# Optimization experiments

Hardware: AMD Instinct MI355X
Metric: run time of the kernel (lower is better)

## Reference

```python
import jax, jax.numpy as jnp
import numpy as np

N_NODES = 100000
N_EDGES = 3200000
IN_DIM = 512
HID_DIM = 16


def spmm(edge_src, edge_dst, edge_weight, feats):
    # out[i] = sum_{(j->i) in E} w_e * feats[j]  (sparse adj @ feats)
    gathered = feats[edge_src] * edge_weight[:, None]  # [E, D]
    return jax.ops.segment_sum(gathered, edge_dst, num_segments=N_NODES)


def setup_inputs() -> dict:
    key = jax.random.key(0)
    ks = jax.random.split(key, 8)
    x = jax.random.normal(ks[0], (N_NODES, IN_DIM), dtype=jnp.float32)
    edge_src = jax.random.randint(ks[1], (N_EDGES,), 0, N_NODES, dtype=jnp.int32)
    edge_dst = jax.random.randint(ks[2], (N_EDGES,), 0, N_NODES, dtype=jnp.int32)
    # normalized adjacency weights (positive, small, like D^-1/2 A D^-1/2 entries)
    edge_weight = jax.random.uniform(ks[3], (N_EDGES,), dtype=jnp.float32) * 0.1
    # Glorot-style init for GraphConvolution weights
    W1 = jax.random.normal(ks[4], (IN_DIM, HID_DIM), dtype=jnp.float32) * (1.0 / np.sqrt(IN_DIM))
    b1 = jnp.zeros((HID_DIM,), dtype=jnp.float32)
    W2 = jax.random.normal(ks[5], (HID_DIM, 1), dtype=jnp.float32) * (1.0 / np.sqrt(HID_DIM))
    b2 = jnp.zeros((1,), dtype=jnp.float32)
    return {"x": x, "edge_src": edge_src, "edge_dst": edge_dst,
            "edge_weight": edge_weight, "W1": W1, "b1": b1, "W2": W2, "b2": b2}


def reference(x, edge_src, edge_dst, edge_weight, W1, b1, W2, b2):
    # Layer 1: GraphConvolution(input_dim -> hidden_dim) + ReLU
    h = spmm(edge_src, edge_dst, edge_weight, x @ W1) + b1  # [N, 16]
    h = jax.nn.relu(h)
    # dropout is identity in eval mode (training=False)
    # Layer 2: GraphConvolution(hidden_dim -> 1)
    out = spmm(edge_src, edge_dst, edge_weight, h @ W2) + b2  # [N, 1]
    return out
```

## Files before the change

kernel.cpp:

```cpp
#include <hip/hip_runtime.h>
#include <hip/hip_fp16.h>

#define N_NODES 100000
#define N_EDGES 3200000
#define IN_DIM  512
#define HID_DIM 16

#define B_BKT   782
#define BKT_SH  7
#define EPB2    5000
#define NBLK2   640
#define CAP_MAX 4608

#define G1_TILES 6250

typedef __attribute__((ext_vector_type(8))) short bf16x8;
typedef __attribute__((ext_vector_type(4))) float f32x4;

__device__ __forceinline__ void atomic_add_f32(float* p, float v) {
    __hip_atomic_fetch_add(p, v, __ATOMIC_RELAXED, __HIP_MEMORY_SCOPE_AGENT);
}
__device__ __forceinline__ int atomic_add_i32(int* p, int v) {
    return __hip_atomic_fetch_add(p, v, __ATOMIC_RELAXED, __HIP_MEMORY_SCOPE_AGENT);
}

__device__ __forceinline__ unsigned short bf16_rne(float f) {
    unsigned u = __float_as_uint(f);
    return (unsigned short)((u + 0x7fffu + ((u >> 16) & 1u)) >> 16);
}

__global__ void z0_init(int* __restrict__ cursor, int cap) {
    int b = blockIdx.x * blockDim.x + threadIdx.x;
    if (b < B_BKT) cursor[b] = b * cap;
}

__global__ __launch_bounds__(256) void g1_xw_mfma(const float* __restrict__ x,
                                                  const float* __restrict__ W1,
                                                  __half* __restrict__ xwh) {
    __shared__ alignas(16) unsigned short whi[16 * 64 * 8];
    __shared__ alignas(16) unsigned short wlo[16 * 64 * 8];
    const int t = threadIdx.x;

    for (int idx = t; idx < 16 * 64 * 8; idx += 256) {
        int c  = idx >> 9;
        int l  = (idx >> 3) & 63;
        int tt = idx & 7;
        int k  = c * 32 + ((l >> 4) << 3) + tt;
        int j  = l & 15;
        float w = W1[k * HID_DIM + j];
        unsigned u = __float_as_uint(w);
        float hif = __uint_as_float(u & 0xffff0000u);
        whi[idx] = (unsigned short)(u >> 16);
        wlo[idx] = bf16_rne(w - hif);
    }
    __syncthreads();

    const int lane = t & 63;
    const int wid  = blockIdx.x * 4 + (t >> 6);
    if (wid >= G1_TILES) return;
    const int row0 = wid * 16;

    const float* xrow = x + (size_t)(row0 + (lane & 15)) * IN_DIM + ((lane >> 4) << 3);
    const unsigned short* whp = &whi[lane * 8];
    const unsigned short* wlp = &wlo[lane * 8];

    f32x4 acc = {0.f, 0.f, 0.f, 0.f};
    float4 p0[2], p1[2];
    p0[0] = *(const float4*)(xrow);
    p1[0] = *(const float4*)(xrow + 4);
    p0[1] = *(const float4*)(xrow + 32);
    p1[1] = *(const float4*)(xrow + 36);
#pragma unroll
    for (int c = 0; c < 16; ++c) {
        const int cur = c & 1;
        float4 n0, n1;
        if (c < 14) {
            n0 = *(const float4*)(xrow + (c + 2) * 32);
            n1 = *(const float4*)(xrow + (c + 2) * 32 + 4);
        }
        float av[8] = {p0[cur].x, p0[cur].y, p0[cur].z, p0[cur].w,
                       p1[cur].x, p1[cur].y, p1[cur].z, p1[cur].w};
        bf16x8 ah, al;
#pragma unroll
        for (int e = 0; e < 8; ++e) {
            unsigned u = __float_as_uint(av[e]);
            ah[e] = (short)(u >> 16);
            float lof = av[e] - __uint_as_float(u & 0xffff0000u);
            al[e] = (short)bf16_rne(lof);
        }
        bf16x8 bh = *(const bf16x8*)(whp + (size_t)c * 512);
        bf16x8 bl = *(const bf16x8*)(wlp + (size_t)c * 512);
        acc = __builtin_amdgcn_mfma_f32_16x16x32_bf16(ah, bh, acc, 0, 0, 0);
        acc = __builtin_amdgcn_mfma_f32_16x16x32_bf16(al, bh, acc, 0, 0, 0);
        acc = __builtin_amdgcn_mfma_f32_16x16x32_bf16(ah, bl, acc, 0, 0, 0);
        if (c < 14) { p0[cur] = n0; p1[cur] = n1; }
    }

    const int n     = lane & 15;
    const int rbase = row0 + ((lane >> 4) << 2);
#pragma unroll
    for (int i = 0; i < 4; ++i)
        xwh[(size_t)(rbase + i) * HID_DIM + n] = __float2half_rn(acc[i]);
}

__global__ __launch_bounds__(512) void s1_bin2(const int* __restrict__ src,
                                               const int* __restrict__ dst,
                                               const float* __restrict__ wgt,
                                               int* __restrict__ cursor,
                                               uint2* __restrict__ rec, int cap) {
    __shared__ uint2 srt[EPB2];
    __shared__ unsigned short bkt[EPB2];
    __shared__ int hist[B_BKT];
    __shared__ int lbase[B_BKT];
    __shared__ int gbase[B_BKT];
    __shared__ int scn[512];
    const int t = threadIdx.x;
    for (int b = t; b < B_BKT; b += 512) hist[b] = 0;
    __syncthreads();

    const int e0 = blockIdx.x * EPB2;
    const int4*   d4 = (const int4*)(dst + e0);
    const int4*   s4 = (const int4*)(src + e0);
    const float4* w4 = (const float4*)(wgt + e0);
    const int NG = EPB2 / 4;

    for (int g = t; g < NG; g += 512) {
        int4 d = d4[g];
        atomicAdd(&hist[d.x >> BKT_SH], 1);
        atomicAdd(&hist[d.y >> BKT_SH], 1);
        atomicAdd(&hist[d.z >> BKT_SH], 1);
        atomicAdd(&hist[d.w >> BKT_SH], 1);
    }
    __syncthreads();

    int c0 = 0, c1 = 0;
    if (t < 391) { c0 = hist[2 * t]; c1 = hist[2 * t + 1]; }
    int s = c0 + c1;
    scn[t] = s;
    __syncthreads();
    for (int off = 1; off < 512; off <<= 1) {
        int v = (t >= off) ? scn[t - off] : 0;
        __syncthreads();
        scn[t] += v;
        __syncthreads();
    }
    int excl = scn[t] - s;
    if (t < 391) {
        lbase[2 * t]     = excl;
        lbase[2 * t + 1] = excl + c0;
    }
    __syncthreads();

    for (int b = t; b < B_BKT; b += 512) {
        int c = hist[b];
        gbase[b] = c > 0 ? atomic_add_i32(&cursor[b], c) : 0;
    }
    __syncthreads();
    for (int b = t; b < B_BKT; b += 512) hist[b] = lbase[b];
    __syncthreads();

    for (int g = t; g < NG; g += 512) {
        int4 d = d4[g];
        int4 sv = s4[g];
        float4 w = w4[g];
        {
            int b = d.x >> BKT_SH;
            int pos = atomicAdd(&hist[b], 1);
            srt[pos] = make_uint2(((unsigned)sv.x << BKT_SH) | (unsigned)(d.x & 127),
                                  __float_as_uint(w.x));
            bkt[pos] = (unsigned short)b;
        }
        {
            int b = d.y >> BKT_SH;
            int pos = atomicAdd(&hist[b], 1);
            srt[pos] = make_uint2(((unsigned)sv.y << BKT_SH) | (unsigned)(d.y & 127),
                                  __float_as_uint(w.y));
            bkt[pos] = (unsigned short)b;
        }
        {
            int b = d.z >> BKT_SH;
            int pos = atomicAdd(&hist[b], 1);
            srt[pos] = make_uint2(((unsigned)sv.z << BKT_SH) | (unsigned)(d.z & 127),
                                  __float_as_uint(w.z));
            bkt[pos] = (unsigned short)b;
        }
        {
            int b = d.w >> BKT_SH;
            int pos = atomicAdd(&hist[b], 1);
            srt[pos] = make_uint2(((unsigned)sv.w << BKT_SH) | (unsigned)(d.w & 127),
                                  __float_as_uint(w.w));
            bkt[pos] = (unsigned short)b;
        }
    }
    __syncthreads();

    for (int i = t; i < EPB2; i += 512) {
        int b = bkt[i];
        rec[gbase[b] + (i - lbase[b])] = srt[i];
    }
}

__global__ __launch_bounds__(512) void s2p4(const int* __restrict__ cursor,
                                            uint2* __restrict__ rec,
                                            int2* __restrict__ row,
                                            const __half* __restrict__ xwh,
                                            const float* __restrict__ b1,
                                            const float* __restrict__ W2,
                                            float* __restrict__ hw, int cap) {
    __shared__ uint2 srt[CAP_MAX];
    __shared__ int ocnt[128], scn[128], cur[128];
    const int t = threadIdx.x;
    const int bkt = blockIdx.x;
    const int e0 = bkt * cap;
    int n = cursor[bkt] - e0;
    n = max(0, min(n, cap));
    if (t < 128) ocnt[t] = 0;
    __syncthreads();
    for (int i = t; i < n; i += 512)
        atomicAdd(&ocnt[rec[e0 + i].x & 127u], 1);
    __syncthreads();
    if (t < 128) scn[t] = ocnt[t];
    __syncthreads();
    for (int off = 1; off < 128; off <<= 1) {
        int v = 0;
        if (t < 128 && t >= off) v = scn[t - off];
        __syncthreads();
        if (t < 128 && t >= off) scn[t] += v;
        __syncthreads();
    }
    if (t < 128) {
        int b = scn[t] - ocnt[t];
        cur[t] = b;
        int node = (bkt << BKT_SH) + t;
        if (node < N_NODES) row[node] = make_int2(e0 + b, ocnt[t]);
    }
    __syncthreads();
    for (int i = t; i < n; i += 512) {
        uint2 r = rec[e0 + i];
        int d = (int)(r.x & 127u);
        int pos = atomicAdd(&cur[d], 1);
        srt[pos] = make_uint2(r.x >> BKT_SH, r.y);
    }
    __syncthreads();
    for (int i = t; i < n; i += 512) rec[e0 + i] = srt[i];
    const int j = t & 15;
    for (int g = (t >> 4); g < 128; g += 32) {
        const int node = (bkt << BKT_SH) + g;
        if (node >= N_NODES) continue;
        int e = scn[g] - ocnt[g];
        const int end = scn[g];
        float acc = 0.0f;
        for (; e + 4 <= end; e += 4) {
            uint2 q0 = srt[e], q1 = srt[e + 1], q2 = srt[e + 2], q3 = srt[e + 3];
            float f0 = __half2float(xwh[(size_t)q0.x * HID_DIM + j]);
            float f1 = __half2float(xwh[(size_t)q1.x * HID_DIM + j]);
            float f2 = __half2float(xwh[(size_t)q2.x * HID_DIM + j]);
            float f3 = __half2float(xwh[(size_t)q3.x * HID_DIM + j]);
            acc += __uint_as_float(q0.y) * f0;
            acc += __uint_as_float(q1.y) * f1;
            acc += __uint_as_float(q2.y) * f2;
            acc += __uint_as_float(q3.y) * f3;
        }
        for (; e < end; ++e) {
            uint2 q = srt[e];
            acc += __uint_as_float(q.y) * __half2float(xwh[(size_t)q.x * HID_DIM + j]);
        }
        float v = fmaxf(acc + b1[j], 0.0f) * W2[j];
        v += __shfl_xor(v, 1);
        v += __shfl_xor(v, 2);
        v += __shfl_xor(v, 4);
        v += __shfl_xor(v, 8);
        if (j == 0) hw[node] = v;
    }
}

__global__ __launch_bounds__(256) void p5_layer2(const int2* __restrict__ row,
                                                 const uint2* __restrict__ rec,
                                                 const float* __restrict__ hwv,
                                                 const float* __restrict__ b2,
                                                 float* __restrict__ out) {
    const int t = threadIdx.x;
    const int node = blockIdx.x * 32 + (t >> 3);
    const int i = t & 7;
    int2 r = row[node];
    const int end = r.x + r.y;
    int k = r.x + i;
    float s = 0.0f;
    for (; k + 24 < end; k += 32) {
        uint2 a = rec[k], b = rec[k + 8], c = rec[k + 16], d = rec[k + 24];
        float ha = hwv[a.x], hb = hwv[b.x], hc = hwv[c.x], hd = hwv[d.x];
        s += __uint_as_float(a.y) * ha + __uint_as_float(b.y) * hb
           + __uint_as_float(c.y) * hc + __uint_as_float(d.y) * hd;
    }
    for (; k < end; k += 8) {
        uint2 a = rec[k];
        s += __uint_as_float(a.y) * hwv[a.x];
    }
    s += __shfl_xor(s, 1);
    s += __shfl_xor(s, 2);
    s += __shfl_xor(s, 4);
    if (i == 0) out[node] = b2[0] + s;
}

__global__ void f0_zero(float* __restrict__ h, const float* __restrict__ b2,
                        float* __restrict__ out) {
    int i = blockIdx.x * blockDim.x + threadIdx.x;
    if (i < N_NODES * HID_DIM) h[i] = 0.0f;
    if (i < N_NODES) out[i] = b2[0];
}
__global__ void k2_spmm1(const int* __restrict__ src, const int* __restrict__ dst,
                         const float* __restrict__ wgt, const __half* __restrict__ xwh,
                         float* __restrict__ h) {
    int t = blockIdx.x * blockDim.x + threadIdx.x;
    int e = t >> 4;
    int j = t & (HID_DIM - 1);
    if (e < N_EDGES) {
        float v = wgt[e] * __half2float(xwh[(size_t)src[e] * HID_DIM + j]);
        atomic_add_f32(&h[(size_t)dst[e] * HID_DIM + j], v);
    }
}
__global__ void k3_act(const float* __restrict__ h, const float* __restrict__ b1,
                       const float* __restrict__ W2, float* __restrict__ hw) {
    int i = blockIdx.x * blockDim.x + threadIdx.x;
    if (i >= N_NODES) return;
    const float4* h4 = (const float4*)(h + (size_t)i * HID_DIM);
    const float4* b4 = (const float4*)b1;
    const float4* w4 = (const float4*)W2;
    float acc = 0.0f;
#pragma unroll
    for (int q = 0; q < HID_DIM / 4; ++q) {
        float4 hv = h4[q]; float4 bv = b4[q]; float4 wv = w4[q];
        acc += fmaxf(hv.x + bv.x, 0.0f) * wv.x;
        acc += fmaxf(hv.y + bv.y, 0.0f) * wv.y;
        acc += fmaxf(hv.z + bv.z, 0.0f) * wv.z;
        acc += fmaxf(hv.w + bv.w, 0.0f) * wv.w;
    }
    hw[i] = acc;
}
__global__ void k4_spmm2(const int* __restrict__ src, const int* __restrict__ dst,
                         const float* __restrict__ wgt, const float* __restrict__ hw,
                         float* __restrict__ out) {
    int e = blockIdx.x * blockDim.x + threadIdx.x;
    if (e < N_EDGES) atomic_add_f32(&out[dst[e]], wgt[e] * hw[src[e]]);
}


extern "C" void kernel_launch(void* const* d_in, const int* in_sizes, int n_in,
                              void* d_out, int out_size, void* d_ws, size_t ws_size,
                              hipStream_t stream) {
    const float* x    = (const float*)d_in[0];
    const int*   esrc = (const int*)  d_in[1];
    const int*   edst = (const int*)  d_in[2];
    const float* ew   = (const float*)d_in[3];
    const float* W1   = (const float*)d_in[4];
    const float* b1   = (const float*)d_in[5];
    const float* W2   = (const float*)d_in[6];
    const float* b2   = (const float*)d_in[7];
    float* out = (float*)d_out;
    char* ws = (char*)d_ws;

    __half* xwh    = (__half*)ws;
    float*  hw     = (float*)(ws + (size_t)N_NODES * HID_DIM * 2);
    int*    cursor = (int*)(hw + N_NODES);
    int2*   row    = (int2*)(((size_t)(cursor + B_BKT) + 7) & ~(size_t)7);
    size_t rec_off = ((size_t)((char*)(row + N_NODES) - ws) + 15) & ~(size_t)15;
    uint2* rec = (uint2*)(ws + rec_off);

    int cap = 0;
    if (ws_size > rec_off) {
        size_t cap_fit = (ws_size - rec_off) / ((size_t)B_BKT * sizeof(uint2));
        cap = (int)(cap_fit < CAP_MAX ? cap_fit : CAP_MAX);
    }

    if (cap >= 4480) {
        z0_init<<<(B_BKT + 255) / 256, 256, 0, stream>>>(cursor, cap);
        g1_xw_mfma<<<(G1_TILES + 3) / 4, 256, 0, stream>>>(x, W1, xwh);
        s1_bin2<<<NBLK2, 512, 0, stream>>>(esrc, edst, ew, cursor, rec, cap);
        s2p4<<<B_BKT, 512, 0, stream>>>(cursor, rec, row, xwh, b1, W2, hw, cap);
        p5_layer2<<<N_NODES / 32, 256, 0, stream>>>(row, rec, hw, b2, out);
    } else {
        __half* f_xwh = (__half*)ws;
        float*  f_h   = (float*)(ws + (size_t)N_NODES * HID_DIM * 2);
        float*  f_hw  = f_h + (size_t)N_NODES * HID_DIM;
        int n = N_NODES * HID_DIM;
        f0_zero<<<(n + 255) / 256, 256, 0, stream>>>(f_h, b2, out);
        g1_xw_mfma<<<(G1_TILES + 3) / 4, 256, 0, stream>>>(x, W1, f_xwh);
        k2_spmm1<<<(N_EDGES * 16) / 256, 256, 0, stream>>>(esrc, edst, ew, f_xwh, f_h);
        k3_act<<<(N_NODES + 255) / 256, 256, 0, stream>>>(f_h, b1, W2, f_hw);
        k4_spmm2<<<(N_EDGES + 255) / 256, 256, 0, stream>>>(esrc, edst, ew, f_hw, out);
    }
}
```

Measured before the change: 406.6 us.

## Merge X·W1 MFMA GEMM and edge binning into one heterogeneous launch

```diff
diff --git a/kernel.cpp b/kernel.cpp
--- a/kernel.cpp
+++ b/kernel.cpp
@@ -13,6 +13,8 @@
 #define CAP_MAX 4608
 
 #define G1_TILES 6250
+#define G1_BLK   782
+#define MERGED_SMEM 61440
 
 typedef __attribute__((ext_vector_type(8))) short bf16x8;
 typedef __attribute__((ext_vector_type(4))) float f32x4;
@@ -32,6 +34,175 @@
 __global__ void z0_init(int* __restrict__ cursor, int cap) {
     int b = blockIdx.x * blockDim.x + threadIdx.x;
     if (b < B_BKT) cursor[b] = b * cap;
+}
+
+__global__ __launch_bounds__(512) void m1_gs(const float* __restrict__ x,
+                                             const float* __restrict__ W1,
+                                             __half* __restrict__ xwh,
+                                             const int* __restrict__ src,
+                                             const int* __restrict__ dst,
+                                             const float* __restrict__ wgt,
+                                             int* __restrict__ cursor,
+                                             uint2* __restrict__ rec, int cap) {
+    extern __shared__ __align__(16) char smem[];
+    const int t = threadIdx.x;
+
+    if (blockIdx.x < NBLK2) {
+        uint2*          srt   = (uint2*)smem;
+        unsigned short* bkt   = (unsigned short*)(smem + 40000);
+        int*            hist  = (int*)(smem + 50000);
+        int*            lbase = (int*)(smem + 53128);
+        int*            gbase = (int*)(smem + 56256);
+        int*            scn   = (int*)(smem + 59384);
+
+        for (int b = t; b < B_BKT; b += 512) hist[b] = 0;
+        __syncthreads();
+
+        const int e0 = blockIdx.x * EPB2;
+        const int4*   d4 = (const int4*)(dst + e0);
+        const int4*   s4 = (const int4*)(src + e0);
+        const float4* w4 = (const float4*)(wgt + e0);
+        const int NG = EPB2 / 4;
+
+        for (int g = t; g < NG; g += 512) {
+            int4 d = d4[g];
+            atomicAdd(&hist[d.x >> BKT_SH], 1);
+            atomicAdd(&hist[d.y >> BKT_SH], 1);
+            atomicAdd(&hist[d.z >> BKT_SH], 1);
+            atomicAdd(&hist[d.w >> BKT_SH], 1);
+        }
+        __syncthreads();
+
+        int c0 = 0, c1 = 0;
+        if (t < 391) { c0 = hist[2 * t]; c1 = hist[2 * t + 1]; }
+        int s = c0 + c1;
+        scn[t] = s;
+        __syncthreads();
+        for (int off = 1; off < 512; off <<= 1) {
+            int v = (t >= off) ? scn[t - off] : 0;
+            __syncthreads();
+            scn[t] += v;
+            __syncthreads();
+        }
+        int excl = scn[t] - s;
+        if (t < 391) {
+            lbase[2 * t]     = excl;
+            lbase[2 * t + 1] = excl + c0;
+        }
+        __syncthreads();
+
+        for (int b = t; b < B_BKT; b += 512) {
+            int c = hist[b];
+            gbase[b] = c > 0 ? atomic_add_i32(&cursor[b], c) : 0;
+        }
+        __syncthreads();
+        for (int b = t; b < B_BKT; b += 512) hist[b] = lbase[b];
+        __syncthreads();
+
+        for (int g = t; g < NG; g += 512) {
+            int4 d = d4[g];
+            int4 sv = s4[g];
+            float4 w = w4[g];
+            {
+                int b = d.x >> BKT_SH;
+                int pos = atomicAdd(&hist[b], 1);
+                srt[pos] = make_uint2(((unsigned)sv.x << BKT_SH) | (unsigned)(d.x & 127),
+                                      __float_as_uint(w.x));
+                bkt[pos] = (unsigned short)b;
+            }
+            {
+                int b = d.y >> BKT_SH;
+                int pos = atomicAdd(&hist[b], 1);
+                srt[pos] = make_uint2(((unsigned)sv.y << BKT_SH) | (unsigned)(d.y & 127),
+                                      __float_as_uint(w.y));
+                bkt[pos] = (unsigned short)b;
+            }
+            {
+                int b = d.z >> BKT_SH;
+                int pos = atomicAdd(&hist[b], 1);
+                srt[pos] = make_uint2(((unsigned)sv.z << BKT_SH) | (unsigned)(d.z & 127),
+                                      __float_as_uint(w.z));
+                bkt[pos] = (unsigned short)b;
+            }
+            {
+                int b = d.w >> BKT_SH;
+                int pos = atomicAdd(&hist[b], 1);
+                srt[pos] = make_uint2(((unsigned)sv.w << BKT_SH) | (unsigned)(d.w & 127),
+                                      __float_as_uint(w.w));
+                bkt[pos] = (unsigned short)b;
+            }
+        }
+        __syncthreads();
+
+        for (int i = t; i < EPB2; i += 512) {
+            int b = bkt[i];
+            rec[gbase[b] + (i - lbase[b])] = srt[i];
+        }
+    } else {
+        unsigned short* whi = (unsigned short*)smem;
+        unsigned short* wlo = (unsigned short*)(smem + 16384);
+
+        for (int idx = t; idx < 16 * 64 * 8; idx += 512) {
+            int c  = idx >> 9;
+            int l  = (idx >> 3) & 63;
+            int tt = idx & 7;
+            int k  = c * 32 + ((l >> 4) << 3) + tt;
+            int j  = l & 15;
+            float w = W1[k * HID_DIM + j];
+            unsigned u = __float_as_uint(w);
+            float hif = __uint_as_float(u & 0xffff0000u);
+            whi[idx] = (unsigned short)(u >> 16);
+            wlo[idx] = bf16_rne(w - hif);
+        }
+        __syncthreads();
+
+        const int lane = t & 63;
+        const int wid  = (blockIdx.x - NBLK2) * 8 + (t >> 6);
+        if (wid >= G1_TILES) return;
+        const int row0 = wid * 16;
+
+        const float* xrow = x + (size_t)(row0 + (lane & 15)) * IN_DIM + ((lane >> 4) << 3);
+        const unsigned short* whp = &whi[lane * 8];
+        const unsigned short* wlp = &wlo[lane * 8];
+
+        f32x4 acc = {0.f, 0.f, 0.f, 0.f};
+        float4 p0[2], p1[2];
+        p0[0] = *(const float4*)(xrow);
+        p1[0] = *(const float4*)(xrow + 4);
+        p0[1] = *(const float4*)(xrow + 32);
+        p1[1] = *(const float4*)(xrow + 36);
+#pragma unroll
+        for (int c = 0; c < 16; ++c) {
+            const int cur = c & 1;
+            float4 n0, n1;
+            if (c < 14) {
+                n0 = *(const float4*)(xrow + (c + 2) * 32);
+                n1 = *(const float4*)(xrow + (c + 2) * 32 + 4);
+            }
+            float av[8] = {p0[cur].x, p0[cur].y, p0[cur].z, p0[cur].w,
+                           p1[cur].x, p1[cur].y, p1[cur].z, p1[cur].w};
+            bf16x8 ah, al;
+#pragma unroll
+            for (int e = 0; e < 8; ++e) {
+                unsigned u = __float_as_uint(av[e]);
+                ah[e] = (short)(u >> 16);
+                float lof = av[e] - __uint_as_float(u & 0xffff0000u);
+                al[e] = (short)bf16_rne(lof);
+            }
+            bf16x8 bh = *(const bf16x8*)(whp + (size_t)c * 512);
+            bf16x8 bl = *(const bf16x8*)(wlp + (size_t)c * 512);
+            acc = __builtin_amdgcn_mfma_f32_16x16x32_bf16(ah, bh, acc, 0, 0, 0);
+            acc = __builtin_amdgcn_mfma_f32_16x16x32_bf16(al, bh, acc, 0, 0, 0);
+            acc = __builtin_amdgcn_mfma_f32_16x16x32_bf16(ah, bl, acc, 0, 0, 0);
+            if (c < 14) { p0[cur] = n0; p1[cur] = n1; }
+        }
+
+        const int n     = lane & 15;
+        const int rbase = row0 + ((lane >> 4) << 2);
+#pragma unroll
+        for (int i = 0; i < 4; ++i)
+            xwh[(size_t)(rbase + i) * HID_DIM + n] = __float2half_rn(acc[i]);
+    }
 }
 
 __global__ __launch_bounds__(256) void g1_xw_mfma(const float* __restrict__ x,
@@ -101,103 +272,6 @@
 #pragma unroll
     for (int i = 0; i < 4; ++i)
         xwh[(size_t)(rbase + i) * HID_DIM + n] = __float2half_rn(acc[i]);
-}
-
-__global__ __launch_bounds__(512) void s1_bin2(const int* __restrict__ src,
-                                               const int* __restrict__ dst,
-                                               const float* __restrict__ wgt,
-                                               int* __restrict__ cursor,
-                                               uint2* __restrict__ rec, int cap) {
-    __shared__ uint2 srt[EPB2];
-    __shared__ unsigned short bkt[EPB2];
-    __shared__ int hist[B_BKT];
-    __shared__ int lbase[B_BKT];
-    __shared__ int gbase[B_BKT];
-    __shared__ int scn[512];
-    const int t = threadIdx.x;
-    for (int b = t; b < B_BKT; b += 512) hist[b] = 0;
-    __syncthreads();
-
-    const int e0 = blockIdx.x * EPB2;
-    const int4*   d4 = (const int4*)(dst + e0);
-    const int4*   s4 = (const int4*)(src + e0);
-    const float4* w4 = (const float4*)(wgt + e0);
-    const int NG = EPB2 / 4;
-
-    for (int g = t; g < NG; g += 512) {
-        int4 d = d4[g];
-        atomicAdd(&hist[d.x >> BKT_SH], 1);
-        atomicAdd(&hist[d.y >> BKT_SH], 1);
-        atomicAdd(&hist[d.z >> BKT_SH], 1);
-        atomicAdd(&hist[d.w >> BKT_SH], 1);
-    }
-    __syncthreads();
-
-    int c0 = 0, c1 = 0;
-    if (t < 391) { c0 = hist[2 * t]; c1 = hist[2 * t + 1]; }
-    int s = c0 + c1;
-    scn[t] = s;
-    __syncthreads();
-    for (int off = 1; off < 512; off <<= 1) {
-        int v = (t >= off) ? scn[t - off] : 0;
-        __syncthreads();
-        scn[t] += v;
-        __syncthreads();
-    }
-    int excl = scn[t] - s;
-    if (t < 391) {
-        lbase[2 * t]     = excl;
-        lbase[2 * t + 1] = excl + c0;
-    }
-    __syncthreads();
-
-    for (int b = t; b < B_BKT; b += 512) {
-        int c = hist[b];
-        gbase[b] = c > 0 ? atomic_add_i32(&cursor[b], c) : 0;
-    }
-    __syncthreads();
-    for (int b = t; b < B_BKT; b += 512) hist[b] = lbase[b];
-    __syncthreads();
-
-    for (int g = t; g < NG; g += 512) {
-        int4 d = d4[g];
-        int4 sv = s4[g];
-        float4 w = w4[g];
-        {
-            int b = d.x >> BKT_SH;
-            int pos = atomicAdd(&hist[b], 1);
-            srt[pos] = make_uint2(((unsigned)sv.x << BKT_SH) | (unsigned)(d.x & 127),
-                                  __float_as_uint(w.x));
-            bkt[pos] = (unsigned short)b;
-        }
-        {
-            int b = d.y >> BKT_SH;
-            int pos = atomicAdd(&hist[b], 1);
-            srt[pos] = make_uint2(((unsigned)sv.y << BKT_SH) | (unsigned)(d.y & 127),
-                                  __float_as_uint(w.y));
-            bkt[pos] = (unsigned short)b;
-        }
-        {
-            int b = d.z >> BKT_SH;
-            int pos = atomicAdd(&hist[b], 1);
-            srt[pos] = make_uint2(((unsigned)sv.z << BKT_SH) | (unsigned)(d.z & 127),
-                                  __float_as_uint(w.z));
-            bkt[pos] = (unsigned short)b;
-        }
-        {
-            int b = d.w >> BKT_SH;
-            int pos = atomicAdd(&hist[b], 1);
-            srt[pos] = make_uint2(((unsigned)sv.w << BKT_SH) | (unsigned)(d.w & 127),
-                                  __float_as_uint(w.w));
-            bkt[pos] = (unsigned short)b;
-        }
-    }
-    __syncthreads();
-
-    for (int i = t; i < EPB2; i += 512) {
-        int b = bkt[i];
-        rec[gbase[b] + (i - lbase[b])] = srt[i];
-    }
 }
 
 __global__ __launch_bounds__(512) void s2p4(const int* __restrict__ cursor,
@@ -374,8 +448,9 @@
 
     if (cap >= 4480) {
         z0_init<<<(B_BKT + 255) / 256, 256, 0, stream>>>(cursor, cap);
-        g1_xw_mfma<<<(G1_TILES + 3) / 4, 256, 0, stream>>>(x, W1, xwh);
-        s1_bin2<<<NBLK2, 512, 0, stream>>>(esrc, edst, ew, cursor, rec, cap);
+        m1_gs<<<NBLK2 + G1_BLK, 512, MERGED_SMEM, stream>>>(x, W1, xwh,
+                                                            esrc, edst, ew,
+                                                            cursor, rec, cap);
         s2p4<<<B_BKT, 512, 0, stream>>>(cursor, rec, row, xwh, b1, W2, hw, cap);
         p5_layer2<<<N_NODES / 32, 256, 0, stream>>>(row, rec, hw, b2, out);
     } else {
```

Measured after the change: 392.9 us. 1.03x faster.
